# Kernel tuning notes

Measured on AMD Instinct MI355X. Metric: run time of the kernel, lower is better.

The kernel has to match this reference:

```python
import jax, jax.numpy as jnp
import numpy as np

B, T, H, W, C = 8, 14, 64, 64, 64
F = 64  # filters (== C, so residual is identity skip)
KH, KW = 3, 3


def _hard_sigmoid(z):
    # Keras hard_sigmoid: clip(0.2*z + 0.5, 0, 1)
    return jnp.clip(0.2 * z + 0.5, 0.0, 1.0)


def _conv_same(inp, k):
    # inp: [B,H,W,Cin], k: [kh,kw,Cin,Cout]
    return jax.lax.conv_general_dilated(
        inp, k, window_strides=(1, 1), padding='SAME',
        dimension_numbers=('NHWC', 'HWIO', 'NHWC'))


def setup_inputs() -> dict:
    key = jax.random.key(0)
    k1, k2, k3, k4 = jax.random.split(key, 4)
    x = jax.random.normal(k1, (B, T, H, W, C), dtype=jnp.float32)
    Wx = jax.random.normal(k2, (KH, KW, C, 4 * F), dtype=jnp.float32) * 0.05
    Wh = jax.random.normal(k3, (KH, KW, F, 4 * F), dtype=jnp.float32) * 0.05
    b = jax.random.normal(k4, (4 * F,), dtype=jnp.float32) * 0.05
    return {'x': x, 'Wx': Wx, 'Wh': Wh, 'b': b}


def reference(x, Wx, Wh, b):
    # ConvLSTM2D (return_sequences=True) + residual add (in_ch == filters).
    # Keras gate order along channel axis: i, f, c(g), o.
    def step(carry, x_t):
        h, c = carry  # each [B,H,W,F]
        z = _conv_same(x_t, Wx) + _conv_same(h, Wh) + b  # [B,H,W,4F]
        zi, zf, zg, zo = jnp.split(z, 4, axis=-1)
        i = _hard_sigmoid(zi)
        f = _hard_sigmoid(zf)
        o = _hard_sigmoid(zo)
        c_new = f * c + i * jnp.tanh(zg)
        h_new = o * jnp.tanh(c_new)
        return (h_new, c_new), h_new

    x_t_first = jnp.moveaxis(x, 1, 0)  # [T,B,H,W,C]
    h0 = jnp.zeros((B, H, W, F), dtype=x.dtype)
    c0 = jnp.zeros((B, H, W, F), dtype=x.dtype)
    _, ys = jax.lax.scan(step, (h0, c0), x_t_first)
    y = jnp.moveaxis(ys, 0, 1)  # [B,T,H,W,F]
    return y + x  # residual skip (in_ch == filters)
```

## Files before the change

### kernel.cpp

```cpp
#include <hip/hip_runtime.h>

#define B_ 8
#define T_ 14
#define HH 64
#define WW 64
#define CC 64
#define FF 64
#define IMG (HH*WW*CC)

typedef __attribute__((ext_vector_type(8))) short short8;
typedef __attribute__((ext_vector_type(4))) float floatx4;

#define WT_OFF   0
#define C_OFF    (1u << 20)
#define H0_OFF   (C_OFF + 8u * 1024 * 1024)
#define H1_OFF   (H0_OFF + 4u * 1024 * 1024)

__device__ __forceinline__ unsigned short bf16_of(float f) {
    unsigned int x = __float_as_uint(f);
    unsigned int r = (x + 0x7FFFu + ((x >> 16) & 1u)) >> 16;
    return (unsigned short)r;
}
__device__ __forceinline__ unsigned int pack2(float a, float b) {
    return (unsigned int)bf16_of(a) | ((unsigned int)bf16_of(b) << 16);
}
__device__ __forceinline__ float hsig(float z) {
    return fminf(fmaxf(fmaf(z, 0.2f, 0.5f), 0.0f), 1.0f);
}
__device__ __forceinline__ float tanh_fast(float v) {
    float e = __expf(2.0f * v);
    return 1.0f - 2.0f / (e + 1.0f);
}

__global__ void repack_weights(const float* __restrict__ Wx,
                               const float* __restrict__ Wh,
                               unsigned short* __restrict__ Wt) {
    int u = blockIdx.x * 256 + threadIdx.x;
    int l  = u & 63;
    int nt = (u >> 6) & 15;
    int g  = (u >> 10) & 1;
    int st = u >> 11;
    const float* W = (st < 9) ? Wx : Wh;
    int tap = (st < 9) ? st : st - 9;
    int n  = nt * 16 + (l & 15);
    int c0 = g * 32 + (l >> 4) * 8;
    unsigned short tmp[8];
    #pragma unroll
    for (int j = 0; j < 8; ++j) {
        tmp[j] = bf16_of(W[(tap * 64 + c0 + j) * 256 + n]);
    }
    *(uint4*)(Wt + (size_t)u * 8) = *(const uint4*)tmp;
}

#define AT(s, r, col, c) ((((s) * 3 + (r)) * 66 + (col)) * 64 + (c))

template<bool FIRST>
__global__ __launch_bounds__(256, 2) void lstm_step_mfma(
    const float* __restrict__ x,
    const unsigned short* __restrict__ Wt,
    const float* __restrict__ bias,
    float* __restrict__ out,
    float* __restrict__ cst,
    const unsigned short* __restrict__ hprev,
    unsigned short* __restrict__ hnext,
    int t)
{
    __shared__ __align__(16) float smem[64 * 260];
    unsigned short* aT = (unsigned short*)smem;

    const int tid = threadIdx.x;
    const int l   = tid & 63;
    const int w   = tid >> 6;
    const int y   = blockIdx.x & 63;
    const int b   = blockIdx.x >> 6;
    const int m16 = l & 15;
    const int q   = l >> 4;

    const float* xbase = x + (size_t)(b * T_ + t) * IMG;

    {
        const int col = (tid >> 2) + 1;
        const int ch  = (tid & 3) * 16;
        #pragma unroll
        for (int r = 0; r < 3; ++r) {
            int iy = y + r - 1;
            uint4 u0 = {0, 0, 0, 0}, u1 = {0, 0, 0, 0};
            if ((unsigned)iy < (unsigned)HH) {
                const float4* s4 = (const float4*)(xbase + iy * (WW * CC)) + tid * 4;
                float4 f0 = s4[0], f1 = s4[1], f2 = s4[2], f3 = s4[3];
                u0.x = pack2(f0.x, f0.y); u0.y = pack2(f0.z, f0.w);
                u0.z = pack2(f1.x, f1.y); u0.w = pack2(f1.z, f1.w);
                u1.x = pack2(f2.x, f2.y); u1.y = pack2(f2.z, f2.w);
                u1.z = pack2(f3.x, f3.y); u1.w = pack2(f3.z, f3.w);
            }
            int off = AT(0, r, col, ch);
            *(uint4*)(aT + off)     = u0;
            *(uint4*)(aT + off + 8) = u1;
        }
        #pragma unroll
        for (int r = 0; r < 3; ++r) {
            int iy = y + r - 1;
            uint4 u0 = {0, 0, 0, 0}, u1 = {0, 0, 0, 0};
            if (!FIRST && (unsigned)iy < (unsigned)HH) {
                const uint4* hp = (const uint4*)(hprev + (size_t)(b * HH + iy) * (WW * CC));
                u0 = hp[tid * 2];
                u1 = hp[tid * 2 + 1];
            }
            int off = AT(1, r, col, ch);
            *(uint4*)(aT + off)     = u0;
            *(uint4*)(aT + off + 8) = u1;
        }
        if (tid < 96) {
            int grp = tid >> 3, l8 = tid & 7;
            int src = grp / 6, rem = grp % 6;
            int r = rem >> 1, colh = (rem & 1) * 65;
            uint4 z = {0, 0, 0, 0};
            *(uint4*)(aT + AT(src, r, colh, l8 * 8)) = z;
        }
    }
    __syncthreads();

    floatx4 acc[4][4];
    #pragma unroll
    for (int nt = 0; nt < 4; ++nt) {
        float bv = bias[w * 64 + nt * 16 + m16];
        #pragma unroll
        for (int mt = 0; mt < 4; ++mt) {
            acc[mt][nt][0] = bv; acc[mt][nt][1] = bv;
            acc[mt][nt][2] = bv; acc[mt][nt][3] = bv;
        }
    }

    const int NSRC = FIRST ? 1 : 2;
    #pragma unroll
    for (int ky = 0; ky < 3; ++ky) {
        #pragma unroll
        for (int kx = 0; kx < 3; ++kx) {
            #pragma unroll
            for (int src = 0; src < NSRC; ++src) {
                #pragma unroll
                for (int g = 0; g < 2; ++g) {
                    short8 af[4];
                    #pragma unroll
                    for (int mt = 0; mt < 4; ++mt) {
                        int col = mt * 16 + m16 + kx;
                        af[mt] = *(const short8*)(aT + AT(src, ky, col, g * 32 + q * 8));
                    }
                    short8 bf[4];
                    int fc = (((src * 9 + ky * 3 + kx) * 2 + g) * 16 + w * 4);
                    #pragma unroll
                    for (int nt = 0; nt < 4; ++nt) {
                        bf[nt] = *(const short8*)(Wt + (size_t)(fc + nt) * 512 + l * 8);
                    }
                    #pragma unroll
                    for (int mt = 0; mt < 4; ++mt) {
                        #pragma unroll
                        for (int nt = 0; nt < 4; ++nt) {
                            acc[mt][nt] = __builtin_amdgcn_mfma_f32_16x16x32_bf16(
                                af[mt], bf[nt], acc[mt][nt], 0, 0, 0);
                        }
                    }
                }
            }
        }
    }

    __syncthreads();
    #pragma unroll
    for (int mt = 0; mt < 4; ++mt) {
        #pragma unroll
        for (int nt = 0; nt < 4; ++nt) {
            int n = w * 64 + nt * 16 + m16;
            #pragma unroll
            for (int r = 0; r < 4; ++r) {
                int m = mt * 16 + q * 4 + r;
                smem[m * 260 + n] = acc[mt][nt][r];
            }
        }
    }
    __syncthreads();

    const int fch   = (tid & 15) * 4;
    const int mbase = tid >> 4;
    const float* xres = xbase + y * (WW * CC);
    float* outrow = out + (size_t)(b * T_ + t) * IMG + y * (WW * CC);
    #pragma unroll
    for (int i = 0; i < 4; ++i) {
        int m = mbase + i * 16;
        const float* zr = smem + m * 260;
        float4 zi = *(const float4*)(zr + fch);
        float4 zf = *(const float4*)(zr + 64 + fch);
        float4 zg = *(const float4*)(zr + 128 + fch);
        float4 zo = *(const float4*)(zr + 192 + fch);
        size_t sidx = (size_t)(b * HH + y) * (WW * CC) + m * 64 + fch;
        float4 cold = {0, 0, 0, 0};
        if (!FIRST) cold = *(const float4*)(cst + sidx);
        float4 xv = *(const float4*)(xres + m * 64 + fch);

        float cn[4], hv[4];
        float zia[4] = {zi.x, zi.y, zi.z, zi.w};
        float zfa[4] = {zf.x, zf.y, zf.z, zf.w};
        float zga[4] = {zg.x, zg.y, zg.z, zg.w};
        float zoa[4] = {zo.x, zo.y, zo.z, zo.w};
        float ca[4]  = {cold.x, cold.y, cold.z, cold.w};
        float xa[4]  = {xv.x, xv.y, xv.z, xv.w};
        #pragma unroll
        for (int k = 0; k < 4; ++k) {
            float ig = hsig(zia[k]);
            float fg = hsig(zfa[k]);
            float gg = tanh_fast(zga[k]);
            float og = hsig(zoa[k]);
            cn[k] = FIRST ? (ig * gg) : fmaf(fg, ca[k], ig * gg);
            hv[k] = og * tanh_fast(cn[k]);
        }
        float4 cnew = {cn[0], cn[1], cn[2], cn[3]};
        *(float4*)(cst + sidx) = cnew;
        ushort4 hb;
        hb.x = bf16_of(hv[0]); hb.y = bf16_of(hv[1]);
        hb.z = bf16_of(hv[2]); hb.w = bf16_of(hv[3]);
        *(ushort4*)(hnext + sidx) = hb;
        float4 yo = {hv[0] + xa[0], hv[1] + xa[1], hv[2] + xa[2], hv[3] + xa[3]};
        *(float4*)(outrow + m * 64 + fch) = yo;
    }
}

extern "C" void kernel_launch(void* const* d_in, const int* in_sizes, int n_in,
                              void* d_out, int out_size, void* d_ws, size_t ws_size,
                              hipStream_t stream) {
    const float* x    = (const float*)d_in[0];
    const float* Wx   = (const float*)d_in[1];
    const float* Wh   = (const float*)d_in[2];
    const float* bias = (const float*)d_in[3];
    float* out = (float*)d_out;

    unsigned short* Wt = (unsigned short*)((char*)d_ws + WT_OFF);
    float* cst         = (float*)((char*)d_ws + C_OFF);
    unsigned short* h0 = (unsigned short*)((char*)d_ws + H0_OFF);
    unsigned short* h1 = (unsigned short*)((char*)d_ws + H1_OFF);

    repack_weights<<<144, 256, 0, stream>>>(Wx, Wh, Wt);

    const int grid = B_ * HH;
    lstm_step_mfma<true><<<grid, 256, 0, stream>>>(x, Wt, bias, out, cst, h0, h0, 0);
    for (int t = 1; t < T_; ++t) {
        unsigned short* hp = (t & 1) ? h0 : h1;
        unsigned short* hn = (t & 1) ? h1 : h0;
        lstm_step_mfma<false><<<grid, 256, 0, stream>>>(x, Wt, bias, out, cst, hp, hn, t);
    }
}
```

Before: 546.4 us.

## Pre-convert x to swizzled bf16, DMA tiles to LDS, fuse gate epilogue in registers

```diff
diff --git a/kernel.cpp b/kernel.cpp
--- a/kernel.cpp
+++ b/kernel.cpp
@@ -5,7 +5,6 @@
 #define HH 64
 #define WW 64
 #define CC 64
-#define FF 64
 #define IMG (HH*WW*CC)
 
 typedef __attribute__((ext_vector_type(8))) short short8;
@@ -15,6 +14,7 @@
 #define C_OFF    (1u << 20)
 #define H0_OFF   (C_OFF + 8u * 1024 * 1024)
 #define H1_OFF   (H0_OFF + 4u * 1024 * 1024)
+#define XBF_OFF  (H1_OFF + 4u * 1024 * 1024)
 
 __device__ __forceinline__ unsigned short bf16_of(float f) {
     unsigned int x = __float_as_uint(f);
@@ -30,6 +30,12 @@
 __device__ __forceinline__ float tanh_fast(float v) {
     float e = __expf(2.0f * v);
     return 1.0f - 2.0f / (e + 1.0f);
+}
+
+__device__ __forceinline__ void dma16(const unsigned short* g, unsigned short* l) {
+    __builtin_amdgcn_global_load_lds(
+        (const __attribute__((address_space(1))) unsigned int*)g,
+        (__attribute__((address_space(3))) unsigned int*)l, 16, 0, 0);
 }
 
 __global__ void repack_weights(const float* __restrict__ Wx,
@@ -52,11 +58,28 @@
     *(uint4*)(Wt + (size_t)u * 8) = *(const uint4*)tmp;
 }
 
+__global__ void convert_x(const float* __restrict__ x,
+                          unsigned short* __restrict__ xbf) {
+    size_t P0 = ((size_t)blockIdx.x * 256 + threadIdx.x) * 8;
+    int d  = (int)(P0 & 4095);
+    int px = d >> 6;
+    int u0 = d & 63;
+    int mask = ((px + 1) & 7) << 3;
+    const float* src = x + (P0 & ~(size_t)4095) + (size_t)(px * 64 + (u0 ^ mask));
+    float4 f0 = *(const float4*)src;
+    float4 f1 = *(const float4*)(src + 4);
+    uint4 o;
+    o.x = pack2(f0.x, f0.y); o.y = pack2(f0.z, f0.w);
+    o.z = pack2(f1.x, f1.y); o.w = pack2(f1.z, f1.w);
+    *(uint4*)(xbf + P0) = o;
+}
+
 #define AT(s, r, col, c) ((((s) * 3 + (r)) * 66 + (col)) * 64 + (c))
 
 template<bool FIRST>
 __global__ __launch_bounds__(256, 2) void lstm_step_mfma(
     const float* __restrict__ x,
+    const unsigned short* __restrict__ xbf,
     const unsigned short* __restrict__ Wt,
     const float* __restrict__ bias,
     float* __restrict__ out,
@@ -65,8 +88,7 @@
     unsigned short* __restrict__ hnext,
     int t)
 {
-    __shared__ __align__(16) float smem[64 * 260];
-    unsigned short* aT = (unsigned short*)smem;
+    __shared__ __align__(16) unsigned short aT[2 * 3 * 66 * 64];
 
     const int tid = threadIdx.x;
     const int l   = tid & 63;
@@ -75,40 +97,39 @@
     const int b   = blockIdx.x >> 6;
     const int m16 = l & 15;
     const int q   = l >> 4;
-
-    const float* xbase = x + (size_t)(b * T_ + t) * IMG;
+    const int ch  = w * 16 + m16;
 
     {
-        const int col = (tid >> 2) + 1;
-        const int ch  = (tid & 3) * 16;
+        const size_t xrowbase = ((size_t)(b * T_ + t) * HH) << 12;
         #pragma unroll
         for (int r = 0; r < 3; ++r) {
             int iy = y + r - 1;
-            uint4 u0 = {0, 0, 0, 0}, u1 = {0, 0, 0, 0};
+            unsigned short* dst = aT + AT(0, r, 1, 0);
             if ((unsigned)iy < (unsigned)HH) {
-                const float4* s4 = (const float4*)(xbase + iy * (WW * CC)) + tid * 4;
-                float4 f0 = s4[0], f1 = s4[1], f2 = s4[2], f3 = s4[3];
-                u0.x = pack2(f0.x, f0.y); u0.y = pack2(f0.z, f0.w);
-                u0.z = pack2(f1.x, f1.y); u0.w = pack2(f1.z, f1.w);
-                u1.x = pack2(f2.x, f2.y); u1.y = pack2(f2.z, f2.w);
-                u1.z = pack2(f3.x, f3.y); u1.w = pack2(f3.z, f3.w);
+                const unsigned short* src = xbf + xrowbase + ((size_t)iy << 12);
+                dma16(src + tid * 8,        dst + (w << 9));
+                dma16(src + tid * 8 + 2048, dst + (w << 9) + 2048);
+            } else {
+                uint4 z = {0, 0, 0, 0};
+                *(uint4*)(dst + tid * 8) = z;
+                *(uint4*)(dst + tid * 8 + 2048) = z;
             }
-            int off = AT(0, r, col, ch);
-            *(uint4*)(aT + off)     = u0;
-            *(uint4*)(aT + off + 8) = u1;
-        }
-        #pragma unroll
-        for (int r = 0; r < 3; ++r) {
-            int iy = y + r - 1;
-            uint4 u0 = {0, 0, 0, 0}, u1 = {0, 0, 0, 0};
-            if (!FIRST && (unsigned)iy < (unsigned)HH) {
-                const uint4* hp = (const uint4*)(hprev + (size_t)(b * HH + iy) * (WW * CC));
-                u0 = hp[tid * 2];
-                u1 = hp[tid * 2 + 1];
+        }
+        if (!FIRST) {
+            #pragma unroll
+            for (int r = 0; r < 3; ++r) {
+                int iy = y + r - 1;
+                unsigned short* dst = aT + AT(1, r, 1, 0);
+                if ((unsigned)iy < (unsigned)HH) {
+                    const unsigned short* src = hprev + (((size_t)(b * HH + iy)) << 12);
+                    dma16(src + tid * 8,        dst + (w << 9));
+                    dma16(src + tid * 8 + 2048, dst + (w << 9) + 2048);
+                } else {
+                    uint4 z = {0, 0, 0, 0};
+                    *(uint4*)(dst + tid * 8) = z;
+                    *(uint4*)(dst + tid * 8 + 2048) = z;
+                }
             }
-            int off = AT(1, r, col, ch);
-            *(uint4*)(aT + off)     = u0;
-            *(uint4*)(aT + off + 8) = u1;
         }
         if (tid < 96) {
             int grp = tid >> 3, l8 = tid & 7;
@@ -123,7 +144,7 @@
     floatx4 acc[4][4];
     #pragma unroll
     for (int nt = 0; nt < 4; ++nt) {
-        float bv = bias[w * 64 + nt * 16 + m16];
+        float bv = bias[nt * 64 + ch];
         #pragma unroll
         for (int mt = 0; mt < 4; ++mt) {
             acc[mt][nt][0] = bv; acc[mt][nt][1] = bv;
@@ -136,21 +157,23 @@
     for (int ky = 0; ky < 3; ++ky) {
         #pragma unroll
         for (int kx = 0; kx < 3; ++kx) {
+            const int swz = ((m16 + kx) & 7) << 3;
             #pragma unroll
             for (int src = 0; src < NSRC; ++src) {
                 #pragma unroll
                 for (int g = 0; g < 2; ++g) {
+                    const int lo = (g * 32 + q * 8) ^ swz;
                     short8 af[4];
                     #pragma unroll
                     for (int mt = 0; mt < 4; ++mt) {
                         int col = mt * 16 + m16 + kx;
-                        af[mt] = *(const short8*)(aT + AT(src, ky, col, g * 32 + q * 8));
+                        af[mt] = *(const short8*)(aT + AT(src, ky, col, lo));
                     }
                     short8 bf[4];
-                    int fc = (((src * 9 + ky * 3 + kx) * 2 + g) * 16 + w * 4);
+                    int fcb = ((src * 9 + ky * 3 + kx) * 2 + g) * 16;
                     #pragma unroll
                     for (int nt = 0; nt < 4; ++nt) {
-                        bf[nt] = *(const short8*)(Wt + (size_t)(fc + nt) * 512 + l * 8);
+                        bf[nt] = *(const short8*)(Wt + (size_t)(fcb + nt * 4 + w) * 512 + l * 8);
                     }
                     #pragma unroll
                     for (int mt = 0; mt < 4; ++mt) {
@@ -165,62 +188,29 @@
         }
     }
 
-    __syncthreads();
+    const size_t rbase = ((size_t)(b * HH + y)) << 12;
+    float* crow = cst + rbase;
+    unsigned short* hrow = hnext + rbase;
+    const float* xr  = x   + (((size_t)(b * T_ + t) * HH + y) << 12);
+    float* orow      = out + (((size_t)(b * T_ + t) * HH + y) << 12);
     #pragma unroll
     for (int mt = 0; mt < 4; ++mt) {
         #pragma unroll
-        for (int nt = 0; nt < 4; ++nt) {
-            int n = w * 64 + nt * 16 + m16;
-            #pragma unroll
-            for (int r = 0; r < 4; ++r) {
-                int m = mt * 16 + q * 4 + r;
-                smem[m * 260 + n] = acc[mt][nt][r];
-            }
-        }
-    }
-    __syncthreads();
-
-    const int fch   = (tid & 15) * 4;
-    const int mbase = tid >> 4;
-    const float* xres = xbase + y * (WW * CC);
-    float* outrow = out + (size_t)(b * T_ + t) * IMG + y * (WW * CC);
-    #pragma unroll
-    for (int i = 0; i < 4; ++i) {
-        int m = mbase + i * 16;
-        const float* zr = smem + m * 260;
-        float4 zi = *(const float4*)(zr + fch);
-        float4 zf = *(const float4*)(zr + 64 + fch);
-        float4 zg = *(const float4*)(zr + 128 + fch);
-        float4 zo = *(const float4*)(zr + 192 + fch);
-        size_t sidx = (size_t)(b * HH + y) * (WW * CC) + m * 64 + fch;
-        float4 cold = {0, 0, 0, 0};
-        if (!FIRST) cold = *(const float4*)(cst + sidx);
-        float4 xv = *(const float4*)(xres + m * 64 + fch);
-
-        float cn[4], hv[4];
-        float zia[4] = {zi.x, zi.y, zi.z, zi.w};
-        float zfa[4] = {zf.x, zf.y, zf.z, zf.w};
-        float zga[4] = {zg.x, zg.y, zg.z, zg.w};
-        float zoa[4] = {zo.x, zo.y, zo.z, zo.w};
-        float ca[4]  = {cold.x, cold.y, cold.z, cold.w};
-        float xa[4]  = {xv.x, xv.y, xv.z, xv.w};
-        #pragma unroll
-        for (int k = 0; k < 4; ++k) {
-            float ig = hsig(zia[k]);
-            float fg = hsig(zfa[k]);
-            float gg = tanh_fast(zga[k]);
-            float og = hsig(zoa[k]);
-            cn[k] = FIRST ? (ig * gg) : fmaf(fg, ca[k], ig * gg);
-            hv[k] = og * tanh_fast(cn[k]);
-        }
-        float4 cnew = {cn[0], cn[1], cn[2], cn[3]};
-        *(float4*)(cst + sidx) = cnew;
-        ushort4 hb;
-        hb.x = bf16_of(hv[0]); hb.y = bf16_of(hv[1]);
-        hb.z = bf16_of(hv[2]); hb.w = bf16_of(hv[3]);
-        *(ushort4*)(hnext + sidx) = hb;
-        float4 yo = {hv[0] + xa[0], hv[1] + xa[1], hv[2] + xa[2], hv[3] + xa[3]};
-        *(float4*)(outrow + m * 64 + fch) = yo;
+        for (int r = 0; r < 4; ++r) {
+            int m   = mt * 16 + q * 4 + r;
+            int idx = m * 64 + ch;
+            float zi = acc[mt][0][r], zf = acc[mt][1][r];
+            float zg = acc[mt][2][r], zo = acc[mt][3][r];
+            float ig = hsig(zi), fg = hsig(zf), og = hsig(zo);
+            float gg = tanh_fast(zg);
+            float cn;
+            if (FIRST) cn = ig * gg;
+            else       cn = fmaf(fg, crow[idx], ig * gg);
+            float hv = og * tanh_fast(cn);
+            crow[idx] = cn;
+            hrow[m * 64 + (ch ^ (((m + 1) & 7) << 3))] = bf16_of(hv);
+            orow[idx] = hv + xr[idx];
+        }
     }
 }
 
@@ -233,18 +223,20 @@
     const float* bias = (const float*)d_in[3];
     float* out = (float*)d_out;
 
-    unsigned short* Wt = (unsigned short*)((char*)d_ws + WT_OFF);
-    float* cst         = (float*)((char*)d_ws + C_OFF);
-    unsigned short* h0 = (unsigned short*)((char*)d_ws + H0_OFF);
-    unsigned short* h1 = (unsigned short*)((char*)d_ws + H1_OFF);
+    unsigned short* Wt  = (unsigned short*)((char*)d_ws + WT_OFF);
+    float* cst          = (float*)((char*)d_ws + C_OFF);
+    unsigned short* h0  = (unsigned short*)((char*)d_ws + H0_OFF);
+    unsigned short* h1  = (unsigned short*)((char*)d_ws + H1_OFF);
+    unsigned short* xbf = (unsigned short*)((char*)d_ws + XBF_OFF);
 
     repack_weights<<<144, 256, 0, stream>>>(Wx, Wh, Wt);
+    convert_x<<<14336, 256, 0, stream>>>(x, xbf);
 
     const int grid = B_ * HH;
-    lstm_step_mfma<true><<<grid, 256, 0, stream>>>(x, Wt, bias, out, cst, h0, h0, 0);
+    lstm_step_mfma<true><<<grid, 256, 0, stream>>>(x, xbf, Wt, bias, out, cst, h0, h0, 0);
     for (int t = 1; t < T_; ++t) {
         unsigned short* hp = (t & 1) ? h0 : h1;
         unsigned short* hn = (t & 1) ? h1 : h0;
-        lstm_step_mfma<false><<<grid, 256, 0, stream>>>(x, Wt, bias, out, cst, hp, hn, t);
-    }
-}
+        lstm_step_mfma<false><<<grid, 256, 0, stream>>>(x, xbf, Wt, bias, out, cst, hp, hn, t);
+    }
+}
```

Measured after the change: 699.2 us. 1.28x slower.
